# Kernel tuning notes

Measured on AMD Instinct MI355X. Metric: run time of the kernel, lower is better.

## Reference

```python
import jax, jax.numpy as jnp
import numpy as np

B, S, E, DK, DV = 8, 2048, 1024, 512, 512
MASK = True


def setup_inputs() -> dict:
    key = jax.random.key(0)
    ks = jax.random.split(key, 12)
    def xavier(k, shape):
        fan_in, fan_out = shape[1], shape[0]
        lim = float(np.sqrt(6.0 / (fan_in + fan_out)))
        return jax.random.uniform(k, shape, jnp.float32, -lim, lim)
    return {
        "x": jax.random.normal(ks[0], (B, S, E), jnp.float32),
        "Wq_w": xavier(ks[1], (DK, E)),
        "Wq_b": jax.random.normal(ks[2], (DK,), jnp.float32) * 0.02,
        "Wk_w": xavier(ks[3], (DK, E)),
        "Wk_b": jax.random.normal(ks[4], (DK,), jnp.float32) * 0.02,
        "Wv_w": xavier(ks[5], (DV, E)),
        "Wv_b": jax.random.normal(ks[6], (DV,), jnp.float32) * 0.02,
        "alphaq": jax.random.normal(ks[7], (S,), jnp.float32) * 0.1,
        "alphav": jax.random.normal(ks[8], (S,), jnp.float32) * 0.1,
        "tokenq": xavier(ks[9], (DK, DK)),
        "tokenv": xavier(ks[10], (DV, DV)),
    }


def reference(x, Wq_w, Wq_b, Wk_w, Wk_b, Wv_w, Wv_b, alphaq, alphav, tokenq, tokenv):
    dk = Wk_w.shape[0]
    seq_len = x.shape[1]
    Q = jnp.einsum("bse,ke->bsk", x, Wq_w) + Wq_b
    K = jnp.einsum("bse,ke->bsk", x, Wk_w) + Wk_b
    V = jnp.einsum("bse,ve->bsv", x, Wv_w) + Wv_b

    # token-aware temperatures: tanh(tokenX @ gelu(X)^T)^T == tanh(gelu(X) @ tokenX^T)
    token_temp_q = jnp.tanh(jnp.einsum("bsj,ij->bsi", jax.nn.gelu(Q, approximate=False), tokenq))
    token_temp_v = jnp.tanh(jnp.einsum("bsj,ij->bsi", jax.nn.gelu(V, approximate=False), tokenv))

    # argmax/gather knobs: [B,S,S] scores -> K_max per query
    attn_map_exps = jnp.einsum("bqk,bsk->bqs", Q, K)
    max_ids = jnp.argmax(attn_map_exps, axis=2)                    # [B,S]
    K_max = jnp.take_along_axis(K, max_ids[:, :, None], axis=1)    # [B,S,DK]
    K_sum = jnp.sum(K, axis=1, keepdims=True)                      # [B,1,DK]
    knobs = jnp.abs(Q * (K_sum - seq_len * K_max))                 # [B,S,DK]

    log_pos = jnp.log(jnp.arange(1, seq_len + 1, dtype=jnp.float32))[None, :, None]  # [1,S,1]
    position_temp_q = 1.0 + jax.nn.sigmoid(alphaq[None, :, None] - knobs) * log_pos
    position_temp_v = 1.0 + jax.nn.sigmoid(alphav)[None, :, None] * log_pos

    gated_Q = (position_temp_q + token_temp_q) * Q
    gated_V = (position_temp_v + token_temp_v) * V

    attention_wts = jnp.einsum("bqk,bsk->bqs", gated_Q, K) / jnp.sqrt(jnp.float32(dk))
    if MASK:
        causal = jnp.triu(jnp.ones((seq_len, seq_len), dtype=bool), k=1)
        attention_wts = jnp.where(causal[None], -jnp.inf, attention_wts)
    attention_scores = jax.nn.softmax(attention_wts.astype(jnp.float32), axis=-1)
    return jnp.einsum("bqs,bsv->bqv", attention_scores, gated_V)
```

## Files before the change

### kernel.cpp

```cpp
#include <hip/hip_runtime.h>
#include <hip/hip_bf16.h>
#include <math.h>

typedef unsigned short u16;
typedef __attribute__((ext_vector_type(8))) short bhalf8;
typedef __attribute__((ext_vector_type(4))) float floatx4;

#define MFMA16(a,b,c) __builtin_amdgcn_mfma_f32_16x16x32_bf16((a),(b),(c),0,0,0)

__device__ __forceinline__ float bf2f(u16 u){ return __uint_as_float(((unsigned)u)<<16); }
__device__ __forceinline__ u16 f2bf(float f){
  unsigned u = __float_as_uint(f);
  u += 0x7fffu + ((u>>16)&1u);
  return (u16)(u>>16);
}
__device__ __forceinline__ float gelu_f(float x){ return 0.5f*x*(1.0f+erff(x*0.70710678118654752f)); }
__device__ __forceinline__ float sigm(float x){ return 1.0f/(1.0f+__expf(-x)); }

__global__ __launch_bounds__(256) void init_counts(int* cnt){
  if (threadIdx.x == 0 && blockIdx.x == 0) *cnt = 0;
}

__global__ __launch_bounds__(256) void cvt_f32_bf16(const float* __restrict__ src,
                                                    u16* __restrict__ dst, int n){
  int i = (blockIdx.x*256 + threadIdx.x)*4;
  if (i >= n) return;
  const float4 v = *(const float4*)(src + i);
  ushort4 o;
  o.x = f2bf(v.x); o.y = f2bf(v.y); o.z = f2bf(v.z); o.w = f2bf(v.w);
  *(ushort4*)(dst + i) = o;
}

__global__ __launch_bounds__(256) void cvt_split(const float* __restrict__ src,
                                                 u16* __restrict__ dsth,
                                                 u16* __restrict__ dstl, int n){
  int i = (blockIdx.x*256 + threadIdx.x)*4;
  if (i >= n) return;
  const float4 v = *(const float4*)(src + i);
  float vv[4] = {v.x, v.y, v.z, v.w};
  ushort4 oh, ol;
  u16 h;
  h = f2bf(vv[0]); oh.x = h; ol.x = f2bf(vv[0] - bf2f(h));
  h = f2bf(vv[1]); oh.y = h; ol.y = f2bf(vv[1] - bf2f(h));
  h = f2bf(vv[2]); oh.z = h; ol.z = f2bf(vv[2] - bf2f(h));
  h = f2bf(vv[3]); oh.w = h; ol.w = f2bf(vv[3] - bf2f(h));
  *(ushort4*)(dsth + i) = oh;
  *(ushort4*)(dstl + i) = ol;
}

__global__ __launch_bounds__(256) void gemm_qkv(
    const u16* __restrict__ xh, const u16* __restrict__ xl,
    const u16* __restrict__ Whh, const u16* __restrict__ Whl,
    const float* __restrict__ bq, const float* __restrict__ bk, const float* __restrict__ bv,
    float* __restrict__ Qf, float* __restrict__ Kf, u16* __restrict__ Vb)
{
  __shared__ __align__(16) u16 Ah[128][72];
  __shared__ __align__(16) u16 Al[128][72];
  __shared__ __align__(16) u16 Bh[128][72];
  __shared__ __align__(16) u16 Bl[128][72];
  const int tid = threadIdx.x;
  const int lane = tid & 63, wid = tid >> 6;
  const int l15 = lane & 15, lg = lane >> 4;
  const int wr = wid >> 1, wc = wid & 1;
  const int m0 = blockIdx.y * 128, n0 = blockIdx.x * 128;
  const int which = n0 >> 9;
  const int nb = n0 & 511;
  const float* bias = (which==0) ? bq : (which==1) ? bk : bv;
  const bool split = (which < 2);

  floatx4 acc[4][4] = {};

  for (int k0 = 0; k0 < 1024; k0 += 64){
    #pragma unroll
    for (int it = 0; it < 4; ++it){
      int e = (tid + it*256)*8;
      int r = e >> 6, c = e & 63;
      size_t ao = (size_t)(m0+r)*1024 + k0 + c;
      size_t bo = (size_t)(n0+r)*1024 + k0 + c;
      *(bhalf8*)&Ah[r][c] = *(const bhalf8*)(xh + ao);
      *(bhalf8*)&Bh[r][c] = *(const bhalf8*)(Whh + bo);
      if (split){
        *(bhalf8*)&Al[r][c] = *(const bhalf8*)(xl + ao);
        *(bhalf8*)&Bl[r][c] = *(const bhalf8*)(Whl + bo);
      }
    }
    __syncthreads();
    #pragma unroll
    for (int kk = 0; kk < 2; ++kk){
      bhalf8 ah[4], bh8[4];
      #pragma unroll
      for (int xx=0; xx<4; xx++){
        ah[xx]  = *(const bhalf8*)&Ah[wr*64 + xx*16 + l15][kk*32 + lg*8];
        bh8[xx] = *(const bhalf8*)&Bh[wc*64 + xx*16 + l15][kk*32 + lg*8];
      }
      if (split){
        bhalf8 al[4], bl8[4];
        #pragma unroll
        for (int xx=0; xx<4; xx++){
          al[xx]  = *(const bhalf8*)&Al[wr*64 + xx*16 + l15][kk*32 + lg*8];
          bl8[xx] = *(const bhalf8*)&Bl[wc*64 + xx*16 + l15][kk*32 + lg*8];
        }
        #pragma unroll
        for (int mi=0;mi<4;mi++)
          #pragma unroll
          for (int ni=0;ni<4;ni++){
            acc[mi][ni] = MFMA16(ah[mi], bh8[ni], acc[mi][ni]);
            acc[mi][ni] = MFMA16(ah[mi], bl8[ni], acc[mi][ni]);
            acc[mi][ni] = MFMA16(al[mi], bh8[ni], acc[mi][ni]);
          }
      } else {
        #pragma unroll
        for (int mi=0;mi<4;mi++)
          #pragma unroll
          for (int ni=0;ni<4;ni++)
            acc[mi][ni] = MFMA16(ah[mi], bh8[ni], acc[mi][ni]);
      }
    }
    __syncthreads();
  }

  #pragma unroll
  for (int mi=0;mi<4;mi++)
    #pragma unroll
    for (int ni=0;ni<4;ni++){
      int cc = nb + wc*64 + ni*16 + l15;
      float bias_v = bias[cc];
      #pragma unroll
      for (int i=0;i<4;i++){
        int row = m0 + wr*64 + mi*16 + lg*4 + i;
        float v = acc[mi][ni][i] + bias_v;
        size_t off = (size_t)row*512 + cc;
        if (which==0){ Qf[off] = v; }
        else if (which==1){ Kf[off] = v; }
        else { Vb[off] = f2bf(v); }
      }
    }
}

__global__ __launch_bounds__(256) void gemm_tanh2(
    const float* __restrict__ Af, const u16* __restrict__ Ab,
    const u16* __restrict__ Bq, const u16* __restrict__ Bv,
    u16* __restrict__ oq, u16* __restrict__ ov)
{
  __shared__ __align__(16) u16 As[128][72];
  __shared__ __align__(16) u16 Bs[128][72];
  const int tid = threadIdx.x;
  const int lane = tid & 63, wid = tid >> 6;
  const int l15 = lane & 15, lg = lane >> 4;
  const int wr = wid >> 1, wc = wid & 1;
  const int m0 = blockIdx.y * 128, n0 = blockIdx.x * 128;
  const int zp = blockIdx.z;
  const u16* B = zp ? Bv : Bq;
  u16* o0 = zp ? ov : oq;

  floatx4 acc[4][4] = {};

  for (int k0 = 0; k0 < 512; k0 += 64){
    #pragma unroll
    for (int it = 0; it < 4; ++it){
      int e = (tid + it*256)*8;
      int r = e >> 6, c = e & 63;
      bhalf8 g;
      if (zp == 0){
        const float* src = Af + (size_t)(m0+r)*512 + k0 + c;
        float4 u0 = *(const float4*)src;
        float4 u1 = *(const float4*)(src+4);
        float vv[8] = {u0.x,u0.y,u0.z,u0.w,u1.x,u1.y,u1.z,u1.w};
        #pragma unroll
        for (int j=0;j<8;j++) g[j] = (short)f2bf(gelu_f(vv[j]));
      } else {
        float4 ra = *(const float4*)(Ab + (size_t)(m0+r)*512 + k0 + c);
        const u16* pu = (const u16*)&ra;
        #pragma unroll
        for (int j=0;j<8;j++) g[j] = (short)f2bf(gelu_f(bf2f(pu[j])));
      }
      *(bhalf8*)&As[r][c] = g;
      *(float4*)&Bs[r][c] = *(const float4*)(B + (size_t)(n0+r)*512 + k0 + c);
    }
    __syncthreads();
    #pragma unroll
    for (int kk = 0; kk < 2; ++kk){
      bhalf8 af[4], bfr[4];
      #pragma unroll
      for (int xx=0;xx<4;xx++) af[xx]  = *(const bhalf8*)&As[wr*64 + xx*16 + l15][kk*32 + lg*8];
      #pragma unroll
      for (int xx=0;xx<4;xx++) bfr[xx] = *(const bhalf8*)&Bs[wc*64 + xx*16 + l15][kk*32 + lg*8];
      #pragma unroll
      for (int mi=0;mi<4;mi++)
        #pragma unroll
        for (int ni=0;ni<4;ni++)
          acc[mi][ni] = MFMA16(af[mi], bfr[ni], acc[mi][ni]);
    }
    __syncthreads();
  }

  #pragma unroll
  for (int mi=0;mi<4;mi++)
    #pragma unroll
    for (int ni=0;ni<4;ni++){
      int coln = n0 + wc*64 + ni*16 + l15;
      #pragma unroll
      for (int i=0;i<4;i++){
        int row = m0 + wr*64 + mi*16 + lg*4 + i;
        o0[(size_t)row*512 + coln] = f2bf(tanhf(acc[mi][ni][i]));
      }
    }
}

__global__ __launch_bounds__(256) void gemm_argmax(
    const float* __restrict__ Qf, const float* __restrict__ Kf,
    float4* __restrict__ part)
{
  __shared__ __align__(16) u16 Ah[128][40];
  __shared__ __align__(16) u16 Al[128][40];
  __shared__ __align__(16) u16 Bh[128][40];
  __shared__ __align__(16) u16 Bl[128][40];
  const int tid = threadIdx.x;
  const int lane = tid & 63, wid = tid >> 6;
  const int l15 = lane & 15, lg = lane >> 4;
  const int wr = wid >> 1, wc = wid & 1;
  const int lin = blockIdx.x + 16*blockIdx.y + 256*blockIdx.z;
  const int swz = (lin & 7)*256 + (lin >> 3);
  const int zb  = swz >> 8;
  const int rem = swz & 255;
  const int m0 = (rem >> 4) * 128;
  const int n0 = (rem & 15) * 128;
  const size_t bo = (size_t)zb * 2048 * 512;

  floatx4 acc[4][4] = {};

  for (int k0 = 0; k0 < 512; k0 += 32){
    #pragma unroll
    for (int it = 0; it < 2; ++it){
      int e = (tid + it*256)*8;
      int r = e >> 5, c = e & 31;
      {
        const float* src = Qf + bo + (size_t)(m0+r)*512 + k0 + c;
        float4 u0 = *(const float4*)src;
        float4 u1 = *(const float4*)(src+4);
        float vv[8] = {u0.x,u0.y,u0.z,u0.w,u1.x,u1.y,u1.z,u1.w};
        bhalf8 h8, l8;
        #pragma unroll
        for (int j=0;j<8;j++){
          u16 h = f2bf(vv[j]); h8[j] = (short)h;
          l8[j] = (short)f2bf(vv[j] - bf2f(h));
        }
        *(bhalf8*)&Ah[r][c] = h8;
        *(bhalf8*)&Al[r][c] = l8;
      }
      {
        const float* src = Kf + bo + (size_t)(n0+r)*512 + k0 + c;
        float4 u0 = *(const float4*)src;
        float4 u1 = *(const float4*)(src+4);
        float vv[8] = {u0.x,u0.y,u0.z,u0.w,u1.x,u1.y,u1.z,u1.w};
        bhalf8 h8, l8;
        #pragma unroll
        for (int j=0;j<8;j++){
          u16 h = f2bf(vv[j]); h8[j] = (short)h;
          l8[j] = (short)f2bf(vv[j] - bf2f(h));
        }
        *(bhalf8*)&Bh[r][c] = h8;
        *(bhalf8*)&Bl[r][c] = l8;
      }
    }
    __syncthreads();
    {
      bhalf8 ah[4], al[4], bh[4], bl[4];
      #pragma unroll
      for (int xx=0;xx<4;xx++){
        ah[xx] = *(const bhalf8*)&Ah[wr*64 + xx*16 + l15][lg*8];
        al[xx] = *(const bhalf8*)&Al[wr*64 + xx*16 + l15][lg*8];
        bh[xx] = *(const bhalf8*)&Bh[wc*64 + xx*16 + l15][lg*8];
        bl[xx] = *(const bhalf8*)&Bl[wc*64 + xx*16 + l15][lg*8];
      }
      #pragma unroll
      for (int mi=0;mi<4;mi++)
        #pragma unroll
        for (int ni=0;ni<4;ni++){
          acc[mi][ni] = MFMA16(ah[mi], bh[ni], acc[mi][ni]);
          acc[mi][ni] = MFMA16(ah[mi], bl[ni], acc[mi][ni]);
          acc[mi][ni] = MFMA16(al[mi], bh[ni], acc[mi][ni]);
        }
    }
    __syncthreads();
  }

  #pragma unroll
  for (int mi=0;mi<4;mi++)
    #pragma unroll
    for (int i=0;i<4;i++){
      float v1 = -INFINITY, v2 = -INFINITY; int i1 = 0x7fffffff;
      #pragma unroll
      for (int ni=0;ni<4;ni++){
        float v = acc[mi][ni][i];
        int col = n0 + wc*64 + ni*16 + l15;
        if (v > v1 || (v == v1 && col < i1)){ v2 = v1; v1 = v; i1 = col; }
        else v2 = fmaxf(v2, v);
      }
      #pragma unroll
      for (int ms=1; ms<16; ms<<=1){
        float w1 = __shfl_xor(v1, ms, 64);
        int   j1 = __shfl_xor(i1, ms, 64);
        float w2 = __shfl_xor(v2, ms, 64);
        if (w1 > v1 || (w1 == v1 && j1 < i1)){ v2 = fmaxf(v1, w2); v1 = w1; i1 = j1; }
        else { v2 = fmaxf(v2, w1); }
      }
      if (l15 == 0){
        int row = m0 + wr*64 + mi*16 + lg*4 + i;
        size_t gm = (size_t)zb*2048 + row;
        part[gm*32 + ((n0>>7)<<1) + wc] = make_float4(v1, __int_as_float(i1), v2, 0.0f);
      }
    }
}

__global__ __launch_bounds__(256) void argmax_reduce(const float4* __restrict__ part,
                                                     int* __restrict__ ids,
                                                     int* __restrict__ list1,
                                                     int* __restrict__ cnt){
  int r = blockIdx.x*256 + threadIdx.x;
  if (r >= 16384) return;
  float v1 = -INFINITY, v2 = -INFINITY; int i1 = 0x7fffffff;
  #pragma unroll
  for (int t=0;t<32;t++){
    float4 p = part[(size_t)r*32 + t];
    float w1 = p.x, w2 = p.z; int j1 = __float_as_int(p.y);
    if (w1 > v1 || (w1 == v1 && j1 < i1)){ v2 = fmaxf(v1, w2); v1 = w1; i1 = j1; }
    else { v2 = fmaxf(v2, w1); }
  }
  ids[r] = i1;
  if (v1 - v2 < 0.02f){
    int k = atomicAdd(cnt, 1);
    if (k < 16384) list1[k] = r;
  }
}

__global__ __launch_bounds__(256) void argmax_fix(
    const float* __restrict__ Qf, const float* __restrict__ Kf,
    const int* __restrict__ list1, const int* __restrict__ cnt,
    int* __restrict__ ids)
{
  __shared__ float q[512];
  __shared__ double rbest[256];
  __shared__ int ridx[256];
  const int tid = threadIdx.x;
  const int n = *cnt;
  for (int j = blockIdx.x; j < n; j += gridDim.x){
    const int r = list1[j];
    const int b = r >> 11;
    __syncthreads();
    for (int d = tid; d < 512; d += 256) q[d] = Qf[(size_t)r*512 + d];
    __syncthreads();
    double best = -1e300; int bi = 0x7fffffff;
    for (int c = 0; c < 8; ++c){
      int key = tid + c*256;
      const float* kr = Kf + ((size_t)b*2048 + key)*512;
      double acc = 0.0;
      for (int e = 0; e < 512; ++e) acc += (double)q[e]*(double)kr[e];
      if (acc > best || (acc == best && key < bi)){ best = acc; bi = key; }
    }
    rbest[tid] = best; ridx[tid] = bi;
    __syncthreads();
    for (int st=128; st>0; st>>=1){
      if (tid < st){
        double ov = rbest[tid+st]; int oi = ridx[tid+st];
        if (ov > rbest[tid] || (ov == rbest[tid] && oi < ridx[tid])){ rbest[tid]=ov; ridx[tid]=oi; }
      }
      __syncthreads();
    }
    if (tid == 0) ids[r] = ridx[0];
    __syncthreads();
  }
}

__global__ __launch_bounds__(256) void ksum_part(const float* __restrict__ Kf,
                                                 float* __restrict__ kpart){
  const int b = blockIdx.x, chunk = blockIdx.y;
  const int tid = threadIdx.x;
  const float* base = Kf + (size_t)b*2048*512 + (size_t)chunk*128*512;
  #pragma unroll
  for (int h = 0; h < 2; ++h){
    int col = tid + h*256;
    double s = 0.0;
    for (int r = 0; r < 128; ++r) s += (double)base[(size_t)r*512 + col];
    kpart[((size_t)b*16 + chunk)*512 + col] = (float)s;
  }
}
__global__ __launch_bounds__(256) void ksum_final(const float* __restrict__ kpart,
                                                  float* __restrict__ Ksum){
  const int b = blockIdx.x >> 1;
  const int col = (blockIdx.x & 1)*256 + threadIdx.x;
  double s = 0.0;
  #pragma unroll
  for (int c = 0; c < 16; ++c) s += (double)kpart[((size_t)b*16 + c)*512 + col];
  Ksum[b*512 + col] = (float)s;
}

__global__ __launch_bounds__(256) void gating_kernel(
    const float* Qf, const float* __restrict__ Kf,
    const u16* __restrict__ V,
    const u16* __restrict__ ttq, const u16* __restrict__ ttv,
    const int* __restrict__ ids, const float* __restrict__ Ksum,
    const float* __restrict__ alphaq, const float* __restrict__ alphav,
    u16* __restrict__ gQh, u16* __restrict__ gQl, float* gVf)
{
  const int m = blockIdx.x;
  const int b = m >> 11, s = m & 2047;
  const int mid = ids[m];
  const float lp = __logf((float)(s+1));
  const float aq = alphaq[s];
  const float pv = 1.0f + sigm(alphav[s])*lp;
  const float qscale = 0.044194173824159220f;
  const size_t ro = (size_t)m*512;
  const size_t ko = ((size_t)b*2048 + mid)*512;
  const int k0 = threadIdx.x*2;

  float2 ks2 = *(const float2*)(Ksum + b*512 + k0);
  float2 q2  = *(const float2*)(Qf + ro + k0);
  float2 km2 = *(const float2*)(Kf + ko + k0);
  ushort2 v2 = *(const ushort2*)(V + ro + k0);
  ushort2 tq2 = *(const ushort2*)(ttq + ro + k0);
  ushort2 tv2 = *(const ushort2*)(ttv + ro + k0);
  ushort2 oqh, oql;
  float2 ov;
  {
    float knob = fabsf(q2.x*(ks2.x - 2048.0f*km2.x));
    float ptq = 1.0f + sigm(aq - knob)*lp;
    float oq = (ptq + bf2f(tq2.x))*q2.x*qscale;
    u16 h = f2bf(oq); oqh.x = h; oql.x = f2bf(oq - bf2f(h));
    ov.x = (pv + bf2f(tv2.x))*bf2f(v2.x);
  }
  {
    float knob = fabsf(q2.y*(ks2.y - 2048.0f*km2.y));
    float ptq = 1.0f + sigm(aq - knob)*lp;
    float oq = (ptq + bf2f(tq2.y))*q2.y*qscale;
    u16 h = f2bf(oq); oqh.y = h; oql.y = f2bf(oq - bf2f(h));
    ov.y = (pv + bf2f(tv2.y))*bf2f(v2.y);
  }
  *(ushort2*)(gQh + ro + k0) = oqh;
  *(ushort2*)(gQl + ro + k0) = oql;
  *(float2*)(gVf + ro + k0) = ov;
}

__global__ __launch_bounds__(256) void transpose_v(const float* __restrict__ src,
                                                   u16* __restrict__ dst){
  __shared__ __align__(16) u16 t[64][72];
  const int b = blockIdx.z;
  const int s0 = blockIdx.x*64, v0 = blockIdx.y*64;
  const float* S = src + (size_t)b*2048*512;
  u16* D = dst + (size_t)b*512*2048;
  const int tid = threadIdx.x;
  #pragma unroll
  for (int it=0; it<2; ++it){
    int e = (tid + it*256)*8;
    int r = e>>6, c = e&63;
    const float* p = S + (size_t)(s0+r)*512 + v0 + c;
    float4 u0 = *(const float4*)p;
    float4 u1 = *(const float4*)(p+4);
    float vv[8] = {u0.x,u0.y,u0.z,u0.w,u1.x,u1.y,u1.z,u1.w};
    bhalf8 o;
    #pragma unroll
    for (int j=0;j<8;j++) o[j] = (short)f2bf(vv[j]);
    *(bhalf8*)&t[r][c] = o;
  }
  __syncthreads();
  #pragma unroll
  for (int it=0; it<2; ++it){
    int e = (tid + it*256)*8;
    int r = e>>6, c = e&63;
    bhalf8 o;
    #pragma unroll
    for (int j=0;j<8;j++) o[j] = (short)t[c+j][r];
    *(bhalf8*)(D + (size_t)(v0+r)*2048 + s0 + c) = o;
  }
}

#define QSW(r,g) ((((g) ^ ((r)&7))) << 3)
__global__ __launch_bounds__(256, 2) void flash3(
    const u16* __restrict__ gQh, const u16* __restrict__ gQl,
    const float* __restrict__ Kf, const u16* __restrict__ gVT,
    float* __restrict__ Out)
{
  const int lin = blockIdx.x + 64*blockIdx.y;
  const int swz = (lin & 7)*64 + (lin >> 3);
  const int b   = swz >> 6;
  const int j   = swz & 63;
  const int qt  = (j & 1) ? (63 - (j >> 1)) : (j >> 1);
  const int q0  = qt * 32;
  const int tid = threadIdx.x, lane = tid & 63, wid = tid >> 6;
  const int l15 = lane & 15, lg = lane >> 4;
  const int wr = wid >> 1, wc = wid & 1;

  __shared__ __align__(16) char smem[74112];
  u16*   qhs = (u16*)smem;
  u16*   khs = (u16*)(smem + 32768);
  u16*   kls = (u16*)(smem + 40960);
  u16*   vss = (u16*)(smem + 49152);
  float* sf  = (float*)(smem + 49152);
  u16*   phs = (u16*)(smem + 65536);
  u16*   pls = (u16*)(smem + 69632);
  float* mstat = (float*)(smem + 73728);
  float* lstat = mstat + 32;
  float* osc   = mstat + 64;

  const u16* Qhb = gQh + ((size_t)b*2048 + q0)*512;
  const float* Kb = Kf + (size_t)b*2048*512;
  const u16* Vtb = gVT + (size_t)b*512*2048;

  #pragma unroll
  for (int it=0; it<8; ++it){
    int e = (tid + it*256)*8;
    int r = e >> 9, c = e & 511;
    bhalf8 hv = *(const bhalf8*)(Qhb + (size_t)r*512 + c);
    *(bhalf8*)&qhs[r*512 + QSW(r, c>>3)] = hv;
  }
  bhalf8 qlr[16];
  {
    const u16* Qlb = gQl + ((size_t)b*2048 + q0 + wr*16 + l15)*512;
    #pragma unroll
    for (int c=0;c<8;c++)
      #pragma unroll
      for (int kk=0;kk<2;kk++)
        qlr[c*2+kk] = *(const bhalf8*)(Qlb + c*64 + kk*32 + lg*8);
  }
  if (tid < 32){ mstat[tid] = -INFINITY; lstat[tid] = 0.0f; }

  floatx4 O[4][2][2] = {};
  __syncthreads();

  auto loadK = [&](int kt, int c, float4* dst){
    #pragma unroll
    for (int it=0; it<2; ++it){
      int e = (tid + it*256)*8;
      int r = e>>6, cc = e&63;
      const float* s = Kb + (size_t)(kt*64+r)*512 + c*64 + cc;
      dst[it*2+0] = *(const float4*)s;
      dst[it*2+1] = *(const float4*)(s+4);
    }
  };
  auto writeK = [&](const float4* src){
    #pragma unroll
    for (int it=0; it<2; ++it){
      int e = (tid + it*256)*8;
      int r = e>>6, cc = e&63;
      float vv[8] = {src[it*2].x,src[it*2].y,src[it*2].z,src[it*2].w,
                     src[it*2+1].x,src[it*2+1].y,src[it*2+1].z,src[it*2+1].w};
      bhalf8 h8, l8;
      #pragma unroll
      for (int jx=0;jx<8;jx++){
        u16 h = f2bf(vv[jx]); h8[jx] = (short)h;
        l8[jx] = (short)f2bf(vv[jx] - bf2f(h));
      }
      int o = r*64 + QSW(r, cc>>3);
      *(bhalf8*)&khs[o] = h8;
      *(bhalf8*)&kls[o] = l8;
    }
  };
  auto loadV = [&](int kt, int vc, bhalf8* dst){
    #pragma unroll
    for (int it=0; it<4; ++it){
      int e = (tid + it*256)*8;
      int r = e>>6, cc = e&63;
      dst[it] = *(const bhalf8*)(Vtb + (size_t)(vc*128+r)*2048 + kt*64 + cc);
    }
  };
  auto writeV = [&](const bhalf8* src){
    #pragma unroll
    for (int it=0; it<4; ++it){
      int e = (tid + it*256)*8;
      int r = e>>6, cc = e&63;
      *(bhalf8*)&vss[r*64 + QSW(r, cc>>3)] = src[it];
    }
  };

  const int qrow = wr*16 + l15;
  const int srow = tid >> 3, seg = tid & 7;

  const int nkt = (q0 + 31)/64 + 1;
  for (int kt = 0; kt < nkt; ++kt){
    floatx4 sacc[2] = {};
    float4 ka[4];
    loadK(kt, 0, ka);
    writeK(ka);
    __syncthreads();
    for (int c = 0; c < 8; ++c){
      float4 kb[4];
      if (c < 7) loadK(kt, c+1, kb);
      #pragma unroll
      for (int kk=0; kk<2; ++kk){
        bhalf8 ah = *(const bhalf8*)&qhs[qrow*512 + QSW(qrow, c*8 + kk*4 + lg)];
        bhalf8 al = qlr[c*2+kk];
        #pragma unroll
        for (int ni=0; ni<2; ++ni){
          int krow = wc*32 + ni*16 + l15;
          int o = krow*64 + QSW(krow, kk*4 + lg);
          bhalf8 bh = *(const bhalf8*)&khs[o];
          bhalf8 bl = *(const bhalf8*)&kls[o];
          sacc[ni] = MFMA16(ah, bh, sacc[ni]);
          sacc[ni] = MFMA16(ah, bl, sacc[ni]);
          sacc[ni] = MFMA16(al, bh, sacc[ni]);
        }
      }
      __syncthreads();
      if (c < 7){
        writeK(kb);
        __syncthreads();
      }
    }
    #pragma unroll
    for (int ni=0; ni<2; ++ni)
      #pragma unroll
      for (int i=0;i<4;i++){
        int row = wr*16 + lg*4 + i;
        int col = wc*32 + ni*16 + l15;
        sf[row*66 + col] = (kt*64 + col <= q0 + row) ? sacc[ni][i] : -INFINITY;
      }
    __syncthreads();
    bhalf8 va[4];
    loadV(kt, 0, va);
    {
      float pv8[8];
      float tmax = -INFINITY;
      #pragma unroll
      for (int jx=0;jx<8;jx++){ pv8[jx] = sf[srow*66 + seg*8 + jx]; tmax = fmaxf(tmax, pv8[jx]); }
      tmax = fmaxf(tmax, __shfl_xor(tmax,1,64));
      tmax = fmaxf(tmax, __shfl_xor(tmax,2,64));
      tmax = fmaxf(tmax, __shfl_xor(tmax,4,64));
      float mo = mstat[srow];
      float mn = fmaxf(mo, tmax);
      float ss = 0.0f;
      bhalf8 h8, l8;
      #pragma unroll
      for (int jx=0;jx<8;jx++){
        float p = __expf(pv8[jx] - mn);
        ss += p;
        u16 hh2 = f2bf(p);
        h8[jx] = (short)hh2;
        l8[jx] = (short)f2bf(p - bf2f(hh2));
      }
      ss += __shfl_xor(ss,1,64);
      ss += __shfl_xor(ss,2,64);
      ss += __shfl_xor(ss,4,64);
      int o = srow*64 + QSW(srow, seg);
      *(bhalf8*)&phs[o] = h8;
      *(bhalf8*)&pls[o] = l8;
      if (seg == 0){
        float sc = __expf(mo - mn);
        lstat[srow] = lstat[srow]*sc + ss;
        mstat[srow] = mn;
        osc[srow] = sc;
      }
    }
    __syncthreads();
    #pragma unroll
    for (int mi=0;mi<2;mi++)
      #pragma unroll
      for (int i=0;i<4;i++){
        float s = osc[mi*16 + lg*4 + i];
        #pragma unroll
        for (int vc=0; vc<4; ++vc)
          #pragma unroll
          for (int ni=0;ni<2;ni++)
            O[vc][mi][ni][i] *= s;
      }
    writeV(va);
    __syncthreads();
    for (int vc = 0; vc < 4; ++vc){
      bhalf8 vb_[4];
      if (vc < 3) loadV(kt, vc+1, vb_);
      #pragma unroll
      for (int kk=0; kk<2; ++kk){
        int gp = kk*4 + lg;
        bhalf8 pah0 = *(const bhalf8*)&phs[l15*64 + QSW(l15, gp)];
        bhalf8 pal0 = *(const bhalf8*)&pls[l15*64 + QSW(l15, gp)];
        bhalf8 pah1 = *(const bhalf8*)&phs[(16+l15)*64 + QSW(16+l15, gp)];
        bhalf8 pal1 = *(const bhalf8*)&pls[(16+l15)*64 + QSW(16+l15, gp)];
        #pragma unroll
        for (int ni=0; ni<2; ++ni){
          int vrow = wid*32 + ni*16 + l15;
          bhalf8 bv_ = *(const bhalf8*)&vss[vrow*64 + QSW(vrow, gp)];
          O[vc][0][ni] = MFMA16(pah0, bv_, O[vc][0][ni]);
          O[vc][0][ni] = MFMA16(pal0, bv_, O[vc][0][ni]);
          O[vc][1][ni] = MFMA16(pah1, bv_, O[vc][1][ni]);
          O[vc][1][ni] = MFMA16(pal1, bv_, O[vc][1][ni]);
        }
      }
      __syncthreads();
      if (vc < 3){
        writeV(vb_);
        __syncthreads();
      }
    }
  }

  #pragma unroll
  for (int vc=0; vc<4; ++vc)
    #pragma unroll
    for (int mi=0;mi<2;mi++)
      #pragma unroll
      for (int i=0;i<4;i++){
        int r = mi*16 + lg*4 + i;
        float inv = 1.0f / lstat[r];
        #pragma unroll
        for (int ni=0;ni<2;ni++){
          int v = vc*128 + wid*32 + ni*16 + l15;
          Out[((size_t)b*2048 + q0 + r)*512 + v] = O[vc][mi][ni][i] * inv;
        }
      }
}

extern "C" void kernel_launch(void* const* d_in, const int* in_sizes, int n_in,
                              void* d_out, int out_size, void* d_ws, size_t ws_size,
                              hipStream_t stream)
{
  const float* x   = (const float*)d_in[0];
  const float* Wq  = (const float*)d_in[1];
  const float* bq  = (const float*)d_in[2];
  const float* Wk  = (const float*)d_in[3];
  const float* bk  = (const float*)d_in[4];
  const float* Wv  = (const float*)d_in[5];
  const float* bv  = (const float*)d_in[6];
  const float* alphaq = (const float*)d_in[7];
  const float* alphav = (const float*)d_in[8];
  const float* tokq = (const float*)d_in[9];
  const float* tokv = (const float*)d_in[10];
  float* out = (float*)d_out;
  char* ws = (char*)d_ws;

  float* Qf  = (float*)(ws + 0);
  float* gVf = Qf;
  float* Kf  = (float*)(ws + 33554432);
  u16* Vb    = (u16*)(ws + 67108864);
  u16* ttq   = (u16*)(ws + 83886080);
  u16* gVT   = ttq;
  u16* ttv   = (u16*)(ws + 100663296);
  u16* xl    = (u16*)(ws + 83886080);
  u16* gQh   = (u16*)(ws + 117440512);
  u16* gQl   = (u16*)(ws + 134217728);
  u16* xh    = (u16*)(ws + 117440512);
  u16* tq_b  = (u16*)(ws + 150994944);
  u16* tv_b  = (u16*)(ws + 151519232);
  int* ids   = (int*)(ws + 152043520);
  float* ksum = (float*)(ws + 152109056);
  float4* part = (float4*)(ws + 152125440);
  u16* Whh   = (u16*)(ws + 152125440);
  u16* Whl   = (u16*)(ws + 155271168);
  int* list1 = (int*)(ws + 160514048);
  int* cnt   = (int*)(ws + 160579584);
  float* kpart = (float*)(ws + 160579840);
  (void)ws_size; (void)in_sizes; (void)n_in; (void)out_size;

  init_counts<<<1,256,0,stream>>>(cnt);
  cvt_f32_bf16<<<256,256,0,stream>>>(tokq, tq_b, 262144);
  cvt_f32_bf16<<<256,256,0,stream>>>(tokv, tv_b, 262144);

  cvt_split<<<16384,256,0,stream>>>(x,  xh, xl, 16777216);
  cvt_split<<<512,256,0,stream>>>(Wq, Whh,            Whl,            524288);
  cvt_split<<<512,256,0,stream>>>(Wk, Whh + 524288,   Whl + 524288,   524288);
  cvt_split<<<512,256,0,stream>>>(Wv, Whh + 1048576,  Whl + 1048576,  524288);

  gemm_qkv<<<dim3(12,128,1),256,0,stream>>>(xh, xl, Whh, Whl, bq, bk, bv, Qf, Kf, Vb);

  gemm_tanh2<<<dim3(4,128,2),256,0,stream>>>(Qf, Vb, tq_b, tv_b, ttq, ttv);

  gemm_argmax<<<dim3(16,16,8),256,0,stream>>>(Qf, Kf, part);
  argmax_reduce<<<64,256,0,stream>>>(part, ids, list1, cnt);
  argmax_fix<<<64,256,0,stream>>>(Qf, Kf, list1, cnt, ids);

  ksum_part<<<dim3(8,16),256,0,stream>>>(Kf, kpart);
  ksum_final<<<16,256,0,stream>>>(kpart, ksum);

  gating_kernel<<<16384,256,0,stream>>>(Qf, Kf, Vb, ttq, ttv, ids, ksum,
                                        alphaq, alphav, gQh, gQl, gVf);

  transpose_v<<<dim3(32,8,8),256,0,stream>>>(gVf, gVT);

  flash3<<<dim3(64,8),256,0,stream>>>(gQh, gQl, Kf, gVT, out);
}
```

Before: 959.0 us.

## Register-prefetch next K tile in GEMMs, split QKV GEMM by precision, remap flash blocks

Adds register double-buffering to the QKV, tanh and argmax GEMMs: the next K-slice is loaded from global memory into registers while MFMAs run on the current shared-memory tile, then written to LDS after a barrier. The QKV GEMM is split into a templated split-precision launch for Q/K and a plain bf16 launch for V. This removes the divergent branch and lets the V launch use less LDS. The flash kernel's block-to-(batch, query tile) mapping is changed so paired causal tiles are balanced per batch. Costs are higher register pressure, an extra barrier per iteration, and one more kernel launch.

```diff
diff --git a/kernel.cpp b/kernel.cpp
--- a/kernel.cpp
+++ b/kernel.cpp
@@ -48,43 +48,64 @@
   *(ushort4*)(dstl + i) = ol;
 }
 
-__global__ __launch_bounds__(256) void gemm_qkv(
+template<int SPLIT>
+__global__ __launch_bounds__(256) void gemm_qkvT(
     const u16* __restrict__ xh, const u16* __restrict__ xl,
     const u16* __restrict__ Whh, const u16* __restrict__ Whl,
     const float* __restrict__ bq, const float* __restrict__ bk, const float* __restrict__ bv,
     float* __restrict__ Qf, float* __restrict__ Kf, u16* __restrict__ Vb)
 {
   __shared__ __align__(16) u16 Ah[128][72];
-  __shared__ __align__(16) u16 Al[128][72];
   __shared__ __align__(16) u16 Bh[128][72];
-  __shared__ __align__(16) u16 Bl[128][72];
+  __shared__ __align__(16) u16 Al[SPLIT?128:1][72];
+  __shared__ __align__(16) u16 Bl[SPLIT?128:1][72];
   const int tid = threadIdx.x;
   const int lane = tid & 63, wid = tid >> 6;
   const int l15 = lane & 15, lg = lane >> 4;
   const int wr = wid >> 1, wc = wid & 1;
-  const int m0 = blockIdx.y * 128, n0 = blockIdx.x * 128;
+  const int m0 = blockIdx.y * 128;
+  const int n0 = blockIdx.x * 128 + (SPLIT ? 0 : 1024);
   const int which = n0 >> 9;
   const int nb = n0 & 511;
   const float* bias = (which==0) ? bq : (which==1) ? bk : bv;
-  const bool split = (which < 2);
 
   floatx4 acc[4][4] = {};
 
-  for (int k0 = 0; k0 < 1024; k0 += 64){
+  bhalf8 RAh[4], RBh[4], RAl[4], RBl[4];
+  auto loadT = [&](int k0){
     #pragma unroll
     for (int it = 0; it < 4; ++it){
       int e = (tid + it*256)*8;
       int r = e >> 6, c = e & 63;
       size_t ao = (size_t)(m0+r)*1024 + k0 + c;
       size_t bo = (size_t)(n0+r)*1024 + k0 + c;
-      *(bhalf8*)&Ah[r][c] = *(const bhalf8*)(xh + ao);
-      *(bhalf8*)&Bh[r][c] = *(const bhalf8*)(Whh + bo);
-      if (split){
-        *(bhalf8*)&Al[r][c] = *(const bhalf8*)(xl + ao);
-        *(bhalf8*)&Bl[r][c] = *(const bhalf8*)(Whl + bo);
-      }
-    }
-    __syncthreads();
+      RAh[it] = *(const bhalf8*)(xh + ao);
+      RBh[it] = *(const bhalf8*)(Whh + bo);
+      if (SPLIT){
+        RAl[it] = *(const bhalf8*)(xl + ao);
+        RBl[it] = *(const bhalf8*)(Whl + bo);
+      }
+    }
+  };
+  auto writeT = [&](){
+    #pragma unroll
+    for (int it = 0; it < 4; ++it){
+      int e = (tid + it*256)*8;
+      int r = e >> 6, c = e & 63;
+      *(bhalf8*)&Ah[r][c] = RAh[it];
+      *(bhalf8*)&Bh[r][c] = RBh[it];
+      if (SPLIT){
+        *(bhalf8*)&Al[r][c] = RAl[it];
+        *(bhalf8*)&Bl[r][c] = RBl[it];
+      }
+    }
+  };
+
+  loadT(0);
+  writeT();
+  __syncthreads();
+  for (int k0 = 0; k0 < 1024; k0 += 64){
+    if (k0 < 960) loadT(k0 + 64);
     #pragma unroll
     for (int kk = 0; kk < 2; ++kk){
       bhalf8 ah[4], bh8[4];
@@ -93,7 +114,7 @@
         ah[xx]  = *(const bhalf8*)&Ah[wr*64 + xx*16 + l15][kk*32 + lg*8];
         bh8[xx] = *(const bhalf8*)&Bh[wc*64 + xx*16 + l15][kk*32 + lg*8];
       }
-      if (split){
+      if (SPLIT){
         bhalf8 al[4], bl8[4];
         #pragma unroll
         for (int xx=0; xx<4; xx++){
@@ -117,6 +138,10 @@
       }
     }
     __syncthreads();
+    if (k0 < 960){
+      writeT();
+      __syncthreads();
+    }
   }
 
   #pragma unroll
@@ -155,29 +180,47 @@
 
   floatx4 acc[4][4] = {};
 
-  for (int k0 = 0; k0 < 512; k0 += 64){
-    #pragma unroll
-    for (int it = 0; it < 4; ++it){
+  float4 RAf[8]; bhalf8 RAb[4]; bhalf8 RB[4];
+  auto loadT = [&](int k0){
+    #pragma unroll
+    for (int it=0; it<4; ++it){
+      int e = (tid + it*256)*8;
+      int r = e >> 6, c = e & 63;
+      if (zp == 0){
+        const float* src = Af + (size_t)(m0+r)*512 + k0 + c;
+        RAf[it*2]   = *(const float4*)src;
+        RAf[it*2+1] = *(const float4*)(src+4);
+      } else {
+        RAb[it] = *(const bhalf8*)(Ab + (size_t)(m0+r)*512 + k0 + c);
+      }
+      RB[it] = *(const bhalf8*)(B + (size_t)(n0+r)*512 + k0 + c);
+    }
+  };
+  auto writeT = [&](){
+    #pragma unroll
+    for (int it=0; it<4; ++it){
       int e = (tid + it*256)*8;
       int r = e >> 6, c = e & 63;
       bhalf8 g;
       if (zp == 0){
-        const float* src = Af + (size_t)(m0+r)*512 + k0 + c;
-        float4 u0 = *(const float4*)src;
-        float4 u1 = *(const float4*)(src+4);
-        float vv[8] = {u0.x,u0.y,u0.z,u0.w,u1.x,u1.y,u1.z,u1.w};
+        float vv[8] = {RAf[it*2].x,RAf[it*2].y,RAf[it*2].z,RAf[it*2].w,
+                       RAf[it*2+1].x,RAf[it*2+1].y,RAf[it*2+1].z,RAf[it*2+1].w};
         #pragma unroll
         for (int j=0;j<8;j++) g[j] = (short)f2bf(gelu_f(vv[j]));
       } else {
-        float4 ra = *(const float4*)(Ab + (size_t)(m0+r)*512 + k0 + c);
-        const u16* pu = (const u16*)&ra;
-        #pragma unroll
-        for (int j=0;j<8;j++) g[j] = (short)f2bf(gelu_f(bf2f(pu[j])));
+        #pragma unroll
+        for (int j=0;j<8;j++) g[j] = (short)f2bf(gelu_f(bf2f((u16)RAb[it][j])));
       }
       *(bhalf8*)&As[r][c] = g;
-      *(float4*)&Bs[r][c] = *(const float4*)(B + (size_t)(n0+r)*512 + k0 + c);
-    }
-    __syncthreads();
+      *(bhalf8*)&Bs[r][c] = RB[it];
+    }
+  };
+
+  loadT(0);
+  writeT();
+  __syncthreads();
+  for (int k0 = 0; k0 < 512; k0 += 64){
+    if (k0 < 448) loadT(k0 + 64);
     #pragma unroll
     for (int kk = 0; kk < 2; ++kk){
       bhalf8 af[4], bfr[4];
@@ -192,6 +235,10 @@
           acc[mi][ni] = MFMA16(af[mi], bfr[ni], acc[mi][ni]);
     }
     __syncthreads();
+    if (k0 < 448){
+      writeT();
+      __syncthreads();
+    }
   }
 
   #pragma unroll
@@ -229,16 +276,28 @@
 
   floatx4 acc[4][4] = {};
 
-  for (int k0 = 0; k0 < 512; k0 += 32){
+  float4 RQ[4], RK[4];
+  auto loadT = [&](int k0){
+    #pragma unroll
+    for (int it = 0; it < 2; ++it){
+      int e = (tid + it*256)*8;
+      int r = e >> 5, c = e & 31;
+      const float* sq = Qf + bo + (size_t)(m0+r)*512 + k0 + c;
+      const float* sk = Kf + bo + (size_t)(n0+r)*512 + k0 + c;
+      RQ[it*2+0] = *(const float4*)sq;
+      RQ[it*2+1] = *(const float4*)(sq+4);
+      RK[it*2+0] = *(const float4*)sk;
+      RK[it*2+1] = *(const float4*)(sk+4);
+    }
+  };
+  auto writeT = [&](){
     #pragma unroll
     for (int it = 0; it < 2; ++it){
       int e = (tid + it*256)*8;
       int r = e >> 5, c = e & 31;
       {
-        const float* src = Qf + bo + (size_t)(m0+r)*512 + k0 + c;
-        float4 u0 = *(const float4*)src;
-        float4 u1 = *(const float4*)(src+4);
-        float vv[8] = {u0.x,u0.y,u0.z,u0.w,u1.x,u1.y,u1.z,u1.w};
+        float vv[8] = {RQ[it*2].x,RQ[it*2].y,RQ[it*2].z,RQ[it*2].w,
+                       RQ[it*2+1].x,RQ[it*2+1].y,RQ[it*2+1].z,RQ[it*2+1].w};
         bhalf8 h8, l8;
         #pragma unroll
         for (int j=0;j<8;j++){
@@ -249,10 +308,8 @@
         *(bhalf8*)&Al[r][c] = l8;
       }
       {
-        const float* src = Kf + bo + (size_t)(n0+r)*512 + k0 + c;
-        float4 u0 = *(const float4*)src;
-        float4 u1 = *(const float4*)(src+4);
-        float vv[8] = {u0.x,u0.y,u0.z,u0.w,u1.x,u1.y,u1.z,u1.w};
+        float vv[8] = {RK[it*2].x,RK[it*2].y,RK[it*2].z,RK[it*2].w,
+                       RK[it*2+1].x,RK[it*2+1].y,RK[it*2+1].z,RK[it*2+1].w};
         bhalf8 h8, l8;
         #pragma unroll
         for (int j=0;j<8;j++){
@@ -263,7 +320,13 @@
         *(bhalf8*)&Bl[r][c] = l8;
       }
     }
-    __syncthreads();
+  };
+
+  loadT(0);
+  writeT();
+  __syncthreads();
+  for (int k0 = 0; k0 < 512; k0 += 32){
+    if (k0 < 480) loadT(k0 + 32);
     {
       bhalf8 ah[4], al[4], bh[4], bl[4];
       #pragma unroll
@@ -283,6 +346,10 @@
         }
     }
     __syncthreads();
+    if (k0 < 480){
+      writeT();
+      __syncthreads();
+    }
   }
 
   #pragma unroll
@@ -480,12 +547,12 @@
     const float* __restrict__ Kf, const u16* __restrict__ gVT,
     float* __restrict__ Out)
 {
-  const int lin = blockIdx.x + 64*blockIdx.y;
-  const int swz = (lin & 7)*64 + (lin >> 3);
-  const int b   = swz >> 6;
-  const int j   = swz & 63;
-  const int qt  = (j & 1) ? (63 - (j >> 1)) : (j >> 1);
-  const int q0  = qt * 32;
+  const int bx = blockIdx.x;
+  const int by = blockIdx.y;
+  const int b  = by;
+  const int hh = (bx & 1) ? (63 - (bx >> 1)) : (bx >> 1);
+  const int qt = (by < 4) ? hh : (63 - hh);
+  const int q0 = qt * 32;
   const int tid = threadIdx.x, lane = tid & 63, wid = tid >> 6;
   const int l15 = lane & 15, lg = lane >> 4;
   const int wr = wid >> 1, wc = wid & 1;
@@ -758,7 +825,8 @@
   cvt_split<<<512,256,0,stream>>>(Wk, Whh + 524288,   Whl + 524288,   524288);
   cvt_split<<<512,256,0,stream>>>(Wv, Whh + 1048576,  Whl + 1048576,  524288);
 
-  gemm_qkv<<<dim3(12,128,1),256,0,stream>>>(xh, xl, Whh, Whl, bq, bk, bv, Qf, Kf, Vb);
+  gemm_qkvT<1><<<dim3(8,128),256,0,stream>>>(xh, xl, Whh, Whl, bq, bk, bv, Qf, Kf, Vb);
+  gemm_qkvT<0><<<dim3(4,128),256,0,stream>>>(xh, xl, Whh, Whl, bq, bk, bv, Qf, Kf, Vb);
 
   gemm_tanh2<<<dim3(4,128,2),256,0,stream>>>(Qf, Vb, tq_b, tv_b, ttq, ttv);
 
```

Result: no change. 971.7 us (+1.3%).
